# Performance work log

Measured on AMD Instinct MI355X. Metric: run time of the kernel, lower is better.

The kernel has to match this reference:

```python
import jax, jax.numpy as jnp
import numpy as np

BATCH, L = 2, 1024
D_MODEL, D_INNER, D_STATE, DT_RANK, K = 2048, 4096, 16, 128, 4


def setup_inputs() -> dict:
    key = jax.random.key(0)
    ks = jax.random.split(key, 9)
    g = lambda i, shape, s: jax.random.normal(ks[i], shape, jnp.float32) * s
    A_log = jnp.log(jnp.broadcast_to(jnp.arange(1, D_STATE + 1, dtype=jnp.float32),
                                     (D_INNER, D_STATE)))
    return {
        "hidden_states": g(0, (BATCH, L, D_MODEL), 1.0),
        "W_in": g(1, (2 * D_INNER, D_MODEL), 0.02),
        "conv_w": g(2, (D_INNER, K), 0.2),
        "conv_b": g(3, (D_INNER,), 0.02),
        "W_x": g(4, (DT_RANK + 2 * D_STATE, D_INNER), 0.02),
        "W_dt": g(5, (D_INNER, DT_RANK), 0.02),
        "b_dt": g(6, (D_INNER,), 0.02),
        "A_log": A_log,
        "D": jnp.ones((D_INNER,), jnp.float32),
        "W_out": g(7, (D_MODEL, D_INNER), 0.02),
        "b_out": g(8, (D_MODEL,), 0.02),
    }


def reference(hidden_states, W_in, conv_w, conv_b, W_x, W_dt, b_dt, A_log, D, W_out, b_out):
    b, l, _ = hidden_states.shape
    # in_proj -> (b, 2*d_inner, l), split into x and gate z
    xz = jnp.einsum('bld,ed->bel', hidden_states, W_in)
    x, z = jnp.split(xz, 2, axis=1)                      # each (b, d_inner, l)
    # conv_state = F.pad(x, (d_conv - l, 0)): keeps the last d_conv timesteps
    conv_state = x[:, :, -K:]
    # causal depthwise conv1d (left pad K-1) + SiLU
    xc = jax.lax.conv_general_dilated(
        x, conv_w[:, None, :], window_strides=(1,), padding=[(K - 1, 0)],
        feature_group_count=D_INNER, dimension_numbers=('NCH', 'OIH', 'NCH'))
    xc = jax.nn.silu(xc + conv_b[None, :, None])         # (b, d_inner, l)
    # x_proj -> dt / B / C
    x_dbl = jnp.einsum('bdl,ed->ble', xc, W_x)           # (b, l, dt_rank+2n)
    dt, Bm, Cm = jnp.split(x_dbl, [DT_RANK, DT_RANK + D_STATE], axis=-1)
    dt = jnp.einsum('blr,dr->bdl', dt, W_dt)             # (b, d_inner, l), no bias here
    delta = jax.nn.softplus(dt + b_dt[None, :, None])    # dt_proj bias folded into softplus
    A = -jnp.exp(A_log)                                  # (d_inner, d_state)

    def step(state, inp):                                # state: (b, d_inner, d_state)
        d_t, b_t, c_t, u_t = inp                         # (b,d), (b,n), (b,n), (b,d)
        dA = jnp.exp(d_t[..., None] * A)                 # (b, d, n)
        state = dA * state + (d_t * u_t)[..., None] * b_t[:, None, :]
        y_t = jnp.einsum('bdn,bn->bd', state, c_t)
        return state, y_t

    xs = (delta.transpose(2, 0, 1),                      # (l, b, d)
          Bm.transpose(1, 0, 2),                         # (l, b, n)
          Cm.transpose(1, 0, 2),
          xc.transpose(2, 0, 1))
    init = jnp.zeros((b, D_INNER, D_STATE), delta.dtype)
    last_state, ys = jax.lax.scan(step, init, xs)
    y = ys.transpose(1, 2, 0) + D[None, :, None] * xc    # (b, d_inner, l) skip term
    y = y * jax.nn.silu(z)                               # gating
    out = jnp.einsum('bdl,ed->ble', y, W_out) + b_out    # (b, l, d_model)
    return out, conv_state, last_state
```

## Files before the change

### kernel.cpp

```cpp
#include <hip/hip_runtime.h>
#include <stdint.h>
#include <stddef.h>

typedef __bf16 bf16;
typedef __attribute__((ext_vector_type(8))) __bf16 bf16x8;
typedef __attribute__((ext_vector_type(4))) float floatx4;

#define GAS __attribute__((address_space(1)))
#define LAS __attribute__((address_space(3)))

__device__ __forceinline__ void async16(const void* g, void* l) {
  __builtin_amdgcn_global_load_lds((const GAS void*)g, (LAS void*)l, 16, 0, 0);
}

__device__ __forceinline__ bf16x8 cvt8(const float* p) {
  floatx4 a = *(const floatx4*)p;
  floatx4 b = *(const floatx4*)(p + 4);
  bf16x8 r;
  r[0] = (bf16)a[0]; r[1] = (bf16)a[1]; r[2] = (bf16)a[2]; r[3] = (bf16)a[3];
  r[4] = (bf16)b[0]; r[5] = (bf16)b[1]; r[6] = (bf16)b[2]; r[7] = (bf16)b[3];
  return r;
}

template <int EPI, int AF, int BF>
__global__ __launch_bounds__(256, 2) void gemm_bt(
    const void* __restrict__ Aptr, const void* __restrict__ Bptr,
    void* __restrict__ Cout, const float* __restrict__ bias,
    int M, int N, int K) {
  __shared__ bf16 As[128 * 32];
  __shared__ bf16 Bs[128 * 32];
  const int tid = threadIdx.x;

  const int rowBase = blockIdx.x * 128;
  const int colBase = blockIdx.y * 128;
  const int kLen = K / gridDim.z;
  const int k0 = blockIdx.z * kLen;
  const int kIters = kLen / 32;

  const int sRow = tid >> 2;
  const int sCol = (tid & 3) << 3;
  const int wave = tid >> 6;
  const int lane = tid & 63;
  const int wm = (wave >> 1) << 6;
  const int wn = (wave & 1) << 6;
  const int lr = lane & 15;
  const int kg = lane >> 4;

  floatx4 acc[4][4] = {};

  for (int kt = 0; kt < kIters; ++kt) {
    const int kk = k0 + kt * 32;
    __syncthreads();
    if constexpr (AF) {
      const float* pa = (const float*)Aptr + (size_t)(rowBase + sRow) * K + kk + sCol;
      *(bf16x8*)&As[tid * 8] = cvt8(pa);
      *(bf16x8*)&As[2048 + tid * 8] = cvt8(pa + (size_t)64 * K);
    } else {
      const bf16* pa = (const bf16*)Aptr + (size_t)(rowBase + sRow) * K + kk + sCol;
      async16(pa, &As[tid * 8]);
      async16(pa + (size_t)64 * K, &As[2048 + tid * 8]);
    }
    if constexpr (BF) {
      const float* pb = (const float*)Bptr + (size_t)(colBase + sRow) * K + kk + sCol;
      *(bf16x8*)&Bs[tid * 8] = cvt8(pb);
      *(bf16x8*)&Bs[2048 + tid * 8] = cvt8(pb + (size_t)64 * K);
    } else {
      const bf16* pb = (const bf16*)Bptr + (size_t)(colBase + sRow) * K + kk + sCol;
      async16(pb, &Bs[tid * 8]);
      async16(pb + (size_t)64 * K, &Bs[2048 + tid * 8]);
    }
    __syncthreads();

    bf16x8 af[4], bg[4];
#pragma unroll
    for (int i = 0; i < 4; ++i)
      af[i] = *(const bf16x8*)&As[(wm + i * 16 + lr) * 32 + kg * 8];
#pragma unroll
    for (int j = 0; j < 4; ++j)
      bg[j] = *(const bf16x8*)&Bs[(wn + j * 16 + lr) * 32 + kg * 8];
#pragma unroll
    for (int i = 0; i < 4; ++i)
#pragma unroll
      for (int j = 0; j < 4; ++j)
        acc[i][j] = __builtin_amdgcn_mfma_f32_16x16x32_bf16(af[i], bg[j],
                                                            acc[i][j], 0, 0, 0);
  }

#pragma unroll
  for (int i = 0; i < 4; ++i) {
#pragma unroll
    for (int j = 0; j < 4; ++j) {
      const int col = colBase + wn + j * 16 + lr;
      float bv = 0.f;
      if constexpr (EPI == 2 || EPI == 3) bv = bias[col];
#pragma unroll
      for (int r = 0; r < 4; ++r) {
        const int row = rowBase + wm + i * 16 + kg * 4 + r;
        const size_t idx = (size_t)row * N + col;
        float v = acc[i][j][r];
        if constexpr (EPI == 0) {
          ((bf16*)Cout)[idx] = (bf16)v;
        } else if constexpr (EPI == 1) {
          atomicAdd((float*)Cout + idx, v);
        } else if constexpr (EPI == 2) {
          v += bv;
          const float t = __expf(v);
          const float sp = (v > 20.f) ? v : __logf(1.f + t);
          ((bf16*)Cout)[idx] = (bf16)sp;
        } else {
          ((float*)Cout)[idx] = v + bv;
        }
      }
    }
  }
}

#define CR0 4194304UL
#define CR1 20971520UL
#define CR2 21495808UL
#define CR3 29884416UL
__global__ __launch_bounds__(256) void cast_all(
    const float* __restrict__ h, const float* __restrict__ wi,
    const float* __restrict__ wd, const float* __restrict__ wo,
    bf16* __restrict__ hb, bf16* __restrict__ wib, bf16* __restrict__ wdb,
    bf16* __restrict__ wob) {
  const size_t g = ((size_t)blockIdx.x * 256 + threadIdx.x) * 8;
  const float* src;
  bf16* dst;
  size_t off;
  if (g < CR0) { src = h; dst = hb; off = g; }
  else if (g < CR1) { src = wi; dst = wib; off = g - CR0; }
  else if (g < CR2) { src = wd; dst = wdb; off = g - CR1; }
  else { src = wo; dst = wob; off = g - CR2; }
  *(bf16x8*)&dst[off] = cvt8(&src[off]);
}

__global__ void wxpad_prep(const float* __restrict__ Wx,
                           bf16* __restrict__ WXPAD) {
  const int idx = blockIdx.x * 256 + threadIdx.x;
  const int row = idx >> 12;
  WXPAD[idx] = (row < 160) ? (bf16)Wx[idx] : (bf16)0.f;
}

__global__ void conv_kernel(const bf16* __restrict__ XZ,
                            const float* __restrict__ conv_w,
                            const float* __restrict__ conv_b,
                            bf16* __restrict__ XC) {
  const int idx = blockIdx.x * 256 + threadIdx.x;
  const int d = idx & 4095;
  const int row = idx >> 12;
  const int l = row & 1023;
  float acc = conv_b[d];
#pragma unroll
  for (int k = 0; k < 4; ++k) {
    if (l - 3 + k >= 0)
      acc += conv_w[d * 4 + k] * (float)XZ[(size_t)(row - 3 + k) * 8192 + d];
  }
  const float s = acc / (1.f + __expf(-acc));
  XC[(size_t)row * 4096 + d] = (bf16)s;
}

__global__ void convstate_kernel(const bf16* __restrict__ XZ,
                                 float* __restrict__ outConv) {
  const int idx = blockIdx.x * 256 + threadIdx.x;
  const int k = idx & 3;
  const int d = (idx >> 2) & 4095;
  const int b = idx >> 14;
  outConv[idx] = (float)XZ[(size_t)(b * 1024 + 1020 + k) * 8192 + d];
}

__global__ void dtcast_kernel(const float* __restrict__ XDBL,
                              bf16* __restrict__ DT) {
  const int idx = blockIdx.x * 256 + threadIdx.x;
  const int row = idx >> 7;
  const int r = idx & 127;
  DT[idx] = (bf16)XDBL[row * 256 + r];
}

#define NCH 32
#define CLEN 32
#define LOG2E 1.44269504088896f

__global__ __launch_bounds__(256) void scan_phase1(
    const bf16* __restrict__ DELTA, const bf16* __restrict__ XC,
    const float* __restrict__ XDBL, const float* __restrict__ A_log,
    bf16* __restrict__ P, bf16* __restrict__ Lc) {
  const int bd = blockIdx.x * 256 + threadIdx.x;
  const int c = blockIdx.y;
  const int b = bd >> 12;
  const int d = bd & 4095;
  float A2[16], st[16], p[16];
#pragma unroll
  for (int n = 0; n < 16; ++n) {
    A2[n] = -__expf(A_log[d * 16 + n]) * LOG2E;
    st[n] = 0.f;
    p[n] = 1.f;
  }
  size_t row = (size_t)b * 1024 + (size_t)c * CLEN;
  for (int t = 0; t < CLEN; ++t, ++row) {
    const float dlt = (float)DELTA[row * 4096 + d];
    const float u = (float)XC[row * 4096 + d];
    const float* __restrict__ Bp = XDBL + row * 256 + 128;
    const float du = dlt * u;
#pragma unroll
    for (int n = 0; n < 16; ++n) {
      const float dA = exp2f(dlt * A2[n]);
      st[n] = dA * st[n] + du * Bp[n];
      p[n] *= dA;
    }
  }
  const size_t o = ((size_t)c * 8192 + bd) * 16;
  bf16x8 pk[2], lk[2];
#pragma unroll
  for (int n = 0; n < 16; ++n) {
    pk[n >> 3][n & 7] = (bf16)p[n];
    lk[n >> 3][n & 7] = (bf16)st[n];
  }
  *(bf16x8*)&P[o] = pk[0];
  *(bf16x8*)&P[o + 8] = pk[1];
  *(bf16x8*)&Lc[o] = lk[0];
  *(bf16x8*)&Lc[o + 8] = lk[1];
}

__global__ __launch_bounds__(256) void scan_phase2(
    const bf16* __restrict__ P, const bf16* __restrict__ Lc,
    float* __restrict__ In, float* __restrict__ lastOut) {
  const int bd = blockIdx.x * 256 + threadIdx.x;
  float st[16] = {};
  for (int c = 0; c < NCH; ++c) {
    const size_t o = ((size_t)c * 8192 + bd) * 16;
    const bf16x8 p0 = *(const bf16x8*)&P[o];
    const bf16x8 p1 = *(const bf16x8*)&P[o + 8];
    const bf16x8 l0 = *(const bf16x8*)&Lc[o];
    const bf16x8 l1 = *(const bf16x8*)&Lc[o + 8];
    floatx4 w[4];
#pragma unroll
    for (int n = 0; n < 16; ++n) w[n >> 2][n & 3] = st[n];
#pragma unroll
    for (int q = 0; q < 4; ++q) *(floatx4*)&In[o + q * 4] = w[q];
#pragma unroll
    for (int n = 0; n < 8; ++n) {
      st[n] = (float)p0[n] * st[n] + (float)l0[n];
      st[8 + n] = (float)p1[n] * st[8 + n] + (float)l1[n];
    }
  }
  const int b = bd >> 12;
  const int d = bd & 4095;
#pragma unroll
  for (int n = 0; n < 16; ++n)
    lastOut[(size_t)b * 65536 + d * 16 + n] = st[n];
}

__global__ __launch_bounds__(256) void scan_phase3(
    const bf16* __restrict__ DELTA, const bf16* __restrict__ XC,
    const bf16* __restrict__ XZ, const float* __restrict__ XDBL,
    const float* __restrict__ A_log, const float* __restrict__ Dp,
    const float* __restrict__ In, bf16* __restrict__ Y) {
  const int bd = blockIdx.x * 256 + threadIdx.x;
  const int c = blockIdx.y;
  const int b = bd >> 12;
  const int d = bd & 4095;
  float A2[16], st[16];
  const size_t o = ((size_t)c * 8192 + bd) * 16;
#pragma unroll
  for (int q = 0; q < 4; ++q) {
    const floatx4 v = *(const floatx4*)&In[o + q * 4];
#pragma unroll
    for (int j = 0; j < 4; ++j) st[q * 4 + j] = v[j];
  }
#pragma unroll
  for (int n = 0; n < 16; ++n)
    A2[n] = -__expf(A_log[d * 16 + n]) * LOG2E;
  const float Dd = Dp[d];
  size_t row = (size_t)b * 1024 + (size_t)c * CLEN;
  for (int t = 0; t < CLEN; ++t, ++row) {
    const float dlt = (float)DELTA[row * 4096 + d];
    const float u = (float)XC[row * 4096 + d];
    const float z = (float)XZ[row * 8192 + 4096 + d];
    const float* __restrict__ Bp = XDBL + row * 256 + 128;
    const float du = dlt * u;
    float y = 0.f;
#pragma unroll
    for (int n = 0; n < 16; ++n) {
      const float dA = exp2f(dlt * A2[n]);
      st[n] = dA * st[n] + du * Bp[n];
      y += st[n] * Bp[16 + n];
    }
    const float sig = 1.f / (1.f + __expf(-z));
    Y[row * 4096 + d] = (bf16)((y + Dd * u) * (z * sig));
  }
}

#define OFF_XZ 0UL
#define OFF_XC 33554432UL
#define OFF_DELTA 50331648UL
#define OFF_Y 83886080UL
#define OFF_XDBL 100663296UL
#define OFF_DT 102760448UL
#define OFF_WXPAD 103284736UL
#define OFF_P 105381888UL
#define OFF_L 113770496UL
#define OFF_HBF 122159104UL
#define OFF_WINBF 130547712UL
#define OFF_WDTBF 164102144UL
#define OFF_WOUTBF 165150720UL
#define WS_NEED_CAST 181927936UL

extern "C" void kernel_launch(void* const* d_in, const int* in_sizes, int n_in,
                              void* d_out, int out_size, void* d_ws,
                              size_t ws_size, hipStream_t stream) {
  const float* hidden = (const float*)d_in[0];
  const float* W_in = (const float*)d_in[1];
  const float* conv_w = (const float*)d_in[2];
  const float* conv_b = (const float*)d_in[3];
  const float* W_x = (const float*)d_in[4];
  const float* W_dt = (const float*)d_in[5];
  const float* b_dt = (const float*)d_in[6];
  const float* A_log = (const float*)d_in[7];
  const float* Dvec = (const float*)d_in[8];
  const float* W_out = (const float*)d_in[9];
  const float* b_out = (const float*)d_in[10];

  char* ws = (char*)d_ws;
  bf16* XZ = (bf16*)(ws + OFF_XZ);
  bf16* XC = (bf16*)(ws + OFF_XC);
  bf16* DELTA = (bf16*)(ws + OFF_DELTA);
  bf16* Y = (bf16*)(ws + OFF_Y);
  float* XDBL = (float*)(ws + OFF_XDBL);
  bf16* DT = (bf16*)(ws + OFF_DT);
  bf16* WXPAD = (bf16*)(ws + OFF_WXPAD);
  bf16* P = (bf16*)(ws + OFF_P);
  bf16* Lc = (bf16*)(ws + OFF_L);

  float* out = (float*)d_out;
  float* out_conv = out + 4194304;
  float* out_last = out + 4227072;
  float* In = out;

  wxpad_prep<<<4096, 256, 0, stream>>>(W_x, WXPAD);
  hipMemsetAsync(XDBL, 0, 2048UL * 256 * 4, stream);

  const bool castOK = ws_size >= WS_NEED_CAST;
  if (castOK) {
    bf16* HBF = (bf16*)(ws + OFF_HBF);
    bf16* WINBF = (bf16*)(ws + OFF_WINBF);
    bf16* WDTBF = (bf16*)(ws + OFF_WDTBF);
    bf16* WOUTBF = (bf16*)(ws + OFF_WOUTBF);
    cast_all<<<14592, 256, 0, stream>>>(hidden, W_in, W_dt, W_out, HBF, WINBF,
                                        WDTBF, WOUTBF);
    gemm_bt<0, 0, 0><<<dim3(16, 64, 1), 256, 0, stream>>>(HBF, WINBF, XZ,
                                                          nullptr, 2048, 8192,
                                                          2048);
    conv_kernel<<<32768, 256, 0, stream>>>(XZ, conv_w, conv_b, XC);
    convstate_kernel<<<128, 256, 0, stream>>>(XZ, out_conv);
    gemm_bt<1, 0, 0><<<dim3(16, 2, 8), 256, 0, stream>>>(XC, WXPAD, XDBL,
                                                         nullptr, 2048, 256,
                                                         4096);
    dtcast_kernel<<<1024, 256, 0, stream>>>(XDBL, DT);
    gemm_bt<2, 0, 0><<<dim3(16, 32, 1), 256, 0, stream>>>(DT, WDTBF, DELTA,
                                                          b_dt, 2048, 4096,
                                                          128);
    scan_phase1<<<dim3(32, NCH), 256, 0, stream>>>(DELTA, XC, XDBL, A_log, P,
                                                   Lc);
    scan_phase2<<<32, 256, 0, stream>>>(P, Lc, In, out_last);
    scan_phase3<<<dim3(32, NCH), 256, 0, stream>>>(DELTA, XC, XZ, XDBL, A_log,
                                                   Dvec, In, Y);
    gemm_bt<3, 0, 0><<<dim3(16, 16, 1), 256, 0, stream>>>(Y, WOUTBF, out, b_out,
                                                          2048, 2048, 4096);
  } else {
    gemm_bt<0, 1, 1><<<dim3(16, 64, 1), 256, 0, stream>>>(hidden, W_in, XZ,
                                                          nullptr, 2048, 8192,
                                                          2048);
    conv_kernel<<<32768, 256, 0, stream>>>(XZ, conv_w, conv_b, XC);
    convstate_kernel<<<128, 256, 0, stream>>>(XZ, out_conv);
    gemm_bt<1, 0, 0><<<dim3(16, 2, 8), 256, 0, stream>>>(XC, WXPAD, XDBL,
                                                         nullptr, 2048, 256,
                                                         4096);
    dtcast_kernel<<<1024, 256, 0, stream>>>(XDBL, DT);
    gemm_bt<2, 0, 1><<<dim3(16, 32, 1), 256, 0, stream>>>(DT, W_dt, DELTA, b_dt,
                                                          2048, 4096, 128);
    scan_phase1<<<dim3(32, NCH), 256, 0, stream>>>(DELTA, XC, XDBL, A_log, P,
                                                   Lc);
    scan_phase2<<<32, 256, 0, stream>>>(P, Lc, In, out_last);
    scan_phase3<<<dim3(32, NCH), 256, 0, stream>>>(DELTA, XC, XZ, XDBL, A_log,
                                                   Dvec, In, Y);
    gemm_bt<3, 0, 1><<<dim3(16, 16, 1), 256, 0, stream>>>(Y, W_out, out, b_out,
                                                          2048, 2048, 4096);
  }
}
```

Before: 544.7 us.

## Fuse prep kernels, drop dtcast, add 64-row GEMM tiles, raise split-K

Merges the weight casts, W_x padding and XDBL zeroing into one prep kernel, and folds the conv_state extraction into the conv kernel. The dt cast kernel is removed: the dt_proj GEMM now reads fp32 XDBL directly with a leading-dimension stride and converts to bf16 on load. A 64-row tile variant is added and used for dt_proj and out_proj to double block counts and improve occupancy. Split-K for x_proj goes from 8 to 16, which means more atomics.

New measurement: 536.5 us. Within noise of the previous version (-1.5%).

```diff
diff --git a/kernel.cpp b/kernel.cpp
--- a/kernel.cpp
+++ b/kernel.cpp
@@ -22,16 +22,16 @@
   return r;
 }
 
-template <int EPI, int AF, int BF>
+template <int EPI, int AF, int BF, int TM>
 __global__ __launch_bounds__(256, 2) void gemm_bt(
     const void* __restrict__ Aptr, const void* __restrict__ Bptr,
     void* __restrict__ Cout, const float* __restrict__ bias,
-    int M, int N, int K) {
-  __shared__ bf16 As[128 * 32];
+    int M, int N, int K, int lda, int ldb) {
+  __shared__ bf16 As[TM * 32];
   __shared__ bf16 Bs[128 * 32];
   const int tid = threadIdx.x;
 
-  const int rowBase = blockIdx.x * 128;
+  const int rowBase = blockIdx.x * TM;
   const int colBase = blockIdx.y * 128;
   const int kLen = K / gridDim.z;
   const int k0 = blockIdx.z * kLen;
@@ -41,55 +41,63 @@
   const int sCol = (tid & 3) << 3;
   const int wave = tid >> 6;
   const int lane = tid & 63;
-  const int wm = (wave >> 1) << 6;
-  const int wn = (wave & 1) << 6;
+  constexpr int MI = 4;
+  constexpr int NJ = (TM == 128) ? 4 : 2;
+  const int wm = (TM == 128) ? ((wave >> 1) << 6) : 0;
+  const int wn = (TM == 128) ? ((wave & 1) << 6) : (wave << 5);
   const int lr = lane & 15;
   const int kg = lane >> 4;
 
-  floatx4 acc[4][4] = {};
+  floatx4 acc[MI][NJ] = {};
 
   for (int kt = 0; kt < kIters; ++kt) {
     const int kk = k0 + kt * 32;
     __syncthreads();
     if constexpr (AF) {
-      const float* pa = (const float*)Aptr + (size_t)(rowBase + sRow) * K + kk + sCol;
+      const float* pa =
+          (const float*)Aptr + (size_t)(rowBase + sRow) * lda + kk + sCol;
       *(bf16x8*)&As[tid * 8] = cvt8(pa);
-      *(bf16x8*)&As[2048 + tid * 8] = cvt8(pa + (size_t)64 * K);
+      if constexpr (TM == 128)
+        *(bf16x8*)&As[2048 + tid * 8] = cvt8(pa + (size_t)64 * lda);
     } else {
-      const bf16* pa = (const bf16*)Aptr + (size_t)(rowBase + sRow) * K + kk + sCol;
+      const bf16* pa =
+          (const bf16*)Aptr + (size_t)(rowBase + sRow) * lda + kk + sCol;
       async16(pa, &As[tid * 8]);
-      async16(pa + (size_t)64 * K, &As[2048 + tid * 8]);
+      if constexpr (TM == 128)
+        async16(pa + (size_t)64 * lda, &As[2048 + tid * 8]);
     }
     if constexpr (BF) {
-      const float* pb = (const float*)Bptr + (size_t)(colBase + sRow) * K + kk + sCol;
+      const float* pb =
+          (const float*)Bptr + (size_t)(colBase + sRow) * ldb + kk + sCol;
       *(bf16x8*)&Bs[tid * 8] = cvt8(pb);
-      *(bf16x8*)&Bs[2048 + tid * 8] = cvt8(pb + (size_t)64 * K);
+      *(bf16x8*)&Bs[2048 + tid * 8] = cvt8(pb + (size_t)64 * ldb);
     } else {
-      const bf16* pb = (const bf16*)Bptr + (size_t)(colBase + sRow) * K + kk + sCol;
+      const bf16* pb =
+          (const bf16*)Bptr + (size_t)(colBase + sRow) * ldb + kk + sCol;
       async16(pb, &Bs[tid * 8]);
-      async16(pb + (size_t)64 * K, &Bs[2048 + tid * 8]);
+      async16(pb + (size_t)64 * ldb, &Bs[2048 + tid * 8]);
     }
     __syncthreads();
 
-    bf16x8 af[4], bg[4];
-#pragma unroll
-    for (int i = 0; i < 4; ++i)
+    bf16x8 af[MI], bg[NJ];
+#pragma unroll
+    for (int i = 0; i < MI; ++i)
       af[i] = *(const bf16x8*)&As[(wm + i * 16 + lr) * 32 + kg * 8];
 #pragma unroll
-    for (int j = 0; j < 4; ++j)
+    for (int j = 0; j < NJ; ++j)
       bg[j] = *(const bf16x8*)&Bs[(wn + j * 16 + lr) * 32 + kg * 8];
 #pragma unroll
-    for (int i = 0; i < 4; ++i)
-#pragma unroll
-      for (int j = 0; j < 4; ++j)
+    for (int i = 0; i < MI; ++i)
+#pragma unroll
+      for (int j = 0; j < NJ; ++j)
         acc[i][j] = __builtin_amdgcn_mfma_f32_16x16x32_bf16(af[i], bg[j],
                                                             acc[i][j], 0, 0, 0);
   }
 
 #pragma unroll
-  for (int i = 0; i < 4; ++i) {
-#pragma unroll
-    for (int j = 0; j < 4; ++j) {
+  for (int i = 0; i < MI; ++i) {
+#pragma unroll
+    for (int j = 0; j < NJ; ++j) {
       const int col = colBase + wn + j * 16 + lr;
       float bv = 0.f;
       if constexpr (EPI == 2 || EPI == 3) bv = bias[col];
@@ -115,24 +123,45 @@
   }
 }
 
-#define CR0 4194304UL
-#define CR1 20971520UL
-#define CR2 21495808UL
-#define CR3 29884416UL
-__global__ __launch_bounds__(256) void cast_all(
+#define PC0 524288UL
+#define PC1 2621440UL
+#define PC2 2686976UL
+#define PC3 3735552UL
+#define PC4 3866624UL
+#define PC5 3932160UL
+__global__ __launch_bounds__(256) void prep_all(
     const float* __restrict__ h, const float* __restrict__ wi,
     const float* __restrict__ wd, const float* __restrict__ wo,
-    bf16* __restrict__ hb, bf16* __restrict__ wib, bf16* __restrict__ wdb,
-    bf16* __restrict__ wob) {
-  const size_t g = ((size_t)blockIdx.x * 256 + threadIdx.x) * 8;
-  const float* src;
-  bf16* dst;
-  size_t off;
-  if (g < CR0) { src = h; dst = hb; off = g; }
-  else if (g < CR1) { src = wi; dst = wib; off = g - CR0; }
-  else if (g < CR2) { src = wd; dst = wdb; off = g - CR1; }
-  else { src = wo; dst = wob; off = g - CR2; }
-  *(bf16x8*)&dst[off] = cvt8(&src[off]);
+    const float* __restrict__ wx, bf16* __restrict__ hb,
+    bf16* __restrict__ wib, bf16* __restrict__ wdb, bf16* __restrict__ wob,
+    bf16* __restrict__ wxp, float* __restrict__ xdbl) {
+  const size_t c = (size_t)blockIdx.x * 256 + threadIdx.x;
+  if (c < PC0) {
+    const size_t e = c * 8;
+    *(bf16x8*)&hb[e] = cvt8(&h[e]);
+  } else if (c < PC1) {
+    const size_t e = (c - PC0) * 8;
+    *(bf16x8*)&wib[e] = cvt8(&wi[e]);
+  } else if (c < PC2) {
+    const size_t e = (c - PC1) * 8;
+    *(bf16x8*)&wdb[e] = cvt8(&wd[e]);
+  } else if (c < PC3) {
+    const size_t e = (c - PC2) * 8;
+    *(bf16x8*)&wob[e] = cvt8(&wo[e]);
+  } else if (c < PC4) {
+    const size_t e = (c - PC3) * 8;
+    if ((e >> 12) < 160) {
+      *(bf16x8*)&wxp[e] = cvt8(&wx[e]);
+    } else {
+      bf16x8 z = {};
+      *(bf16x8*)&wxp[e] = z;
+    }
+  } else {
+    const size_t e = (c - PC4) * 8;
+    floatx4 z = {};
+    *(floatx4*)&xdbl[e] = z;
+    *(floatx4*)&xdbl[e + 4] = z;
+  }
 }
 
 __global__ void wxpad_prep(const float* __restrict__ Wx,
@@ -145,7 +174,8 @@
 __global__ void conv_kernel(const bf16* __restrict__ XZ,
                             const float* __restrict__ conv_w,
                             const float* __restrict__ conv_b,
-                            bf16* __restrict__ XC) {
+                            bf16* __restrict__ XC,
+                            float* __restrict__ outConv) {
   const int idx = blockIdx.x * 256 + threadIdx.x;
   const int d = idx & 4095;
   const int row = idx >> 12;
@@ -158,23 +188,12 @@
   }
   const float s = acc / (1.f + __expf(-acc));
   XC[(size_t)row * 4096 + d] = (bf16)s;
-}
-
-__global__ void convstate_kernel(const bf16* __restrict__ XZ,
-                                 float* __restrict__ outConv) {
-  const int idx = blockIdx.x * 256 + threadIdx.x;
-  const int k = idx & 3;
-  const int d = (idx >> 2) & 4095;
-  const int b = idx >> 14;
-  outConv[idx] = (float)XZ[(size_t)(b * 1024 + 1020 + k) * 8192 + d];
-}
-
-__global__ void dtcast_kernel(const float* __restrict__ XDBL,
-                              bf16* __restrict__ DT) {
-  const int idx = blockIdx.x * 256 + threadIdx.x;
-  const int row = idx >> 7;
-  const int r = idx & 127;
-  DT[idx] = (bf16)XDBL[row * 256 + r];
+  if (idx < 32768) {
+    const int k = idx & 3;
+    const int dd = (idx >> 2) & 4095;
+    const int b = idx >> 14;
+    outConv[idx] = (float)XZ[(size_t)(b * 1024 + 1020 + k) * 8192 + dd];
+  }
 }
 
 #define NCH 32
@@ -296,7 +315,6 @@
 #define OFF_DELTA 50331648UL
 #define OFF_Y 83886080UL
 #define OFF_XDBL 100663296UL
-#define OFF_DT 102760448UL
 #define OFF_WXPAD 103284736UL
 #define OFF_P 105381888UL
 #define OFF_L 113770496UL
@@ -327,7 +345,6 @@
   bf16* DELTA = (bf16*)(ws + OFF_DELTA);
   bf16* Y = (bf16*)(ws + OFF_Y);
   float* XDBL = (float*)(ws + OFF_XDBL);
-  bf16* DT = (bf16*)(ws + OFF_DT);
   bf16* WXPAD = (bf16*)(ws + OFF_WXPAD);
   bf16* P = (bf16*)(ws + OFF_P);
   bf16* Lc = (bf16*)(ws + OFF_L);
@@ -336,9 +353,6 @@
   float* out_conv = out + 4194304;
   float* out_last = out + 4227072;
   float* In = out;
-
-  wxpad_prep<<<4096, 256, 0, stream>>>(W_x, WXPAD);
-  hipMemsetAsync(XDBL, 0, 2048UL * 256 * 4, stream);
 
   const bool castOK = ws_size >= WS_NEED_CAST;
   if (castOK) {
@@ -346,45 +360,38 @@
     bf16* WINBF = (bf16*)(ws + OFF_WINBF);
     bf16* WDTBF = (bf16*)(ws + OFF_WDTBF);
     bf16* WOUTBF = (bf16*)(ws + OFF_WOUTBF);
-    cast_all<<<14592, 256, 0, stream>>>(hidden, W_in, W_dt, W_out, HBF, WINBF,
-                                        WDTBF, WOUTBF);
-    gemm_bt<0, 0, 0><<<dim3(16, 64, 1), 256, 0, stream>>>(HBF, WINBF, XZ,
-                                                          nullptr, 2048, 8192,
-                                                          2048);
-    conv_kernel<<<32768, 256, 0, stream>>>(XZ, conv_w, conv_b, XC);
-    convstate_kernel<<<128, 256, 0, stream>>>(XZ, out_conv);
-    gemm_bt<1, 0, 0><<<dim3(16, 2, 8), 256, 0, stream>>>(XC, WXPAD, XDBL,
-                                                         nullptr, 2048, 256,
-                                                         4096);
-    dtcast_kernel<<<1024, 256, 0, stream>>>(XDBL, DT);
-    gemm_bt<2, 0, 0><<<dim3(16, 32, 1), 256, 0, stream>>>(DT, WDTBF, DELTA,
-                                                          b_dt, 2048, 4096,
-                                                          128);
+    prep_all<<<15360, 256, 0, stream>>>(hidden, W_in, W_dt, W_out, W_x, HBF,
+                                        WINBF, WDTBF, WOUTBF, WXPAD, XDBL);
+    gemm_bt<0, 0, 0, 128><<<dim3(16, 64, 1), 256, 0, stream>>>(
+        HBF, WINBF, XZ, nullptr, 2048, 8192, 2048, 2048, 2048);
+    conv_kernel<<<32768, 256, 0, stream>>>(XZ, conv_w, conv_b, XC, out_conv);
+    gemm_bt<1, 0, 0, 128><<<dim3(16, 2, 16), 256, 0, stream>>>(
+        XC, WXPAD, XDBL, nullptr, 2048, 256, 4096, 4096, 4096);
+    gemm_bt<2, 1, 0, 64><<<dim3(32, 32, 1), 256, 0, stream>>>(
+        XDBL, WDTBF, DELTA, b_dt, 2048, 4096, 128, 256, 128);
     scan_phase1<<<dim3(32, NCH), 256, 0, stream>>>(DELTA, XC, XDBL, A_log, P,
                                                    Lc);
     scan_phase2<<<32, 256, 0, stream>>>(P, Lc, In, out_last);
     scan_phase3<<<dim3(32, NCH), 256, 0, stream>>>(DELTA, XC, XZ, XDBL, A_log,
                                                    Dvec, In, Y);
-    gemm_bt<3, 0, 0><<<dim3(16, 16, 1), 256, 0, stream>>>(Y, WOUTBF, out, b_out,
-                                                          2048, 2048, 4096);
+    gemm_bt<3, 0, 0, 64><<<dim3(32, 16, 1), 256, 0, stream>>>(
+        Y, WOUTBF, out, b_out, 2048, 2048, 4096, 4096, 4096);
   } else {
-    gemm_bt<0, 1, 1><<<dim3(16, 64, 1), 256, 0, stream>>>(hidden, W_in, XZ,
-                                                          nullptr, 2048, 8192,
-                                                          2048);
-    conv_kernel<<<32768, 256, 0, stream>>>(XZ, conv_w, conv_b, XC);
-    convstate_kernel<<<128, 256, 0, stream>>>(XZ, out_conv);
-    gemm_bt<1, 0, 0><<<dim3(16, 2, 8), 256, 0, stream>>>(XC, WXPAD, XDBL,
-                                                         nullptr, 2048, 256,
-                                                         4096);
-    dtcast_kernel<<<1024, 256, 0, stream>>>(XDBL, DT);
-    gemm_bt<2, 0, 1><<<dim3(16, 32, 1), 256, 0, stream>>>(DT, W_dt, DELTA, b_dt,
-                                                          2048, 4096, 128);
+    wxpad_prep<<<4096, 256, 0, stream>>>(W_x, WXPAD);
+    hipMemsetAsync(XDBL, 0, 2048UL * 256 * 4, stream);
+    gemm_bt<0, 1, 1, 128><<<dim3(16, 64, 1), 256, 0, stream>>>(
+        hidden, W_in, XZ, nullptr, 2048, 8192, 2048, 2048, 2048);
+    conv_kernel<<<32768, 256, 0, stream>>>(XZ, conv_w, conv_b, XC, out_conv);
+    gemm_bt<1, 0, 0, 128><<<dim3(16, 2, 16), 256, 0, stream>>>(
+        XC, WXPAD, XDBL, nullptr, 2048, 256, 4096, 4096, 4096);
+    gemm_bt<2, 1, 1, 64><<<dim3(32, 32, 1), 256, 0, stream>>>(
+        XDBL, W_dt, DELTA, b_dt, 2048, 4096, 128, 256, 128);
     scan_phase1<<<dim3(32, NCH), 256, 0, stream>>>(DELTA, XC, XDBL, A_log, P,
                                                    Lc);
     scan_phase2<<<32, 256, 0, stream>>>(P, Lc, In, out_last);
     scan_phase3<<<dim3(32, NCH), 256, 0, stream>>>(DELTA, XC, XZ, XDBL, A_log,
                                                    Dvec, In, Y);
-    gemm_bt<3, 0, 1><<<dim3(16, 16, 1), 256, 0, stream>>>(Y, W_out, out, b_out,
-                                                          2048, 2048, 4096);
-  }
-}
+    gemm_bt<3, 0, 1, 64><<<dim3(32, 16, 1), 256, 0, stream>>>(
+        Y, W_out, out, b_out, 2048, 2048, 4096, 4096, 4096);
+  }
+}
```
